# Kernel tuning notes

Measured on AMD Instinct MI355X. Metric: run time of the kernel, lower is better.

Reference implementation:

```python
import jax, jax.numpy as jnp
import numpy as np

NEG_SLOPE = 0.2  # PyG GATConv default negative_slope


def _gat_conv(x, edge_index, W, att_src, att_dst, bias, heads, out_ch, concat):
    """PyG-style GATConv with add_self_loops=False, shared src/dst lin.
    x: [N, F_in], edge_index: [2, E] (row 0 = src j, row 1 = dst i).
    W: [F_in, heads*out_ch]; att_src/att_dst: [heads, out_ch]; bias: [heads*out_ch] or [out_ch].
    """
    N = x.shape[0]
    src, dst = edge_index[0], edge_index[1]
    h = (x @ W).reshape(N, heads, out_ch)                      # [N, H, C]
    a_src = jnp.einsum('nhc,hc->nh', h, att_src)               # [N, H]
    a_dst = jnp.einsum('nhc,hc->nh', h, att_dst)               # [N, H]
    e = a_src[src] + a_dst[dst]                                # [E, H]
    e = jnp.where(e > 0, e, NEG_SLOPE * e)                     # leaky_relu
    # segment softmax over edges sharing the same destination
    m = jax.ops.segment_max(e, dst, num_segments=N)            # [N, H]
    e = jnp.exp(e - m[dst])                                    # [E, H]
    s = jax.ops.segment_sum(e, dst, num_segments=N)            # [N, H]
    alpha = e / (s[dst] + 1e-16)                               # [E, H]
    msg = h[src] * alpha[:, :, None]                           # [E, H, C]
    out = jax.ops.segment_sum(msg, dst, num_segments=N)        # [N, H, C]
    if concat:
        out = out.reshape(N, heads * out_ch)
    else:
        out = out.mean(axis=1)
    return out + bias


def setup_inputs() -> dict:
    key = jax.random.key(0)
    ks = jax.random.split(key, 12)
    N, E = 100000, 1600000
    dinp, dhid, dout, heads = 128, 32, 128, 4
    x = jax.random.normal(ks[0], (N, dinp), dtype=jnp.float32)
    a = jax.random.randint(ks[1], (2, E), 0, N, dtype=jnp.int64)
    s1 = 1.0 / np.sqrt(dinp)
    s2 = 1.0 / np.sqrt(dhid * heads)
    return {
        'x': x,
        'a': a,
        'W1': jax.random.normal(ks[2], (dinp, heads * dhid), dtype=jnp.float32) * s1,
        'att_src1': jax.random.normal(ks[3], (heads, dhid), dtype=jnp.float32) * s1,
        'att_dst1': jax.random.normal(ks[4], (heads, dhid), dtype=jnp.float32) * s1,
        'b1': jnp.zeros((heads * dhid,), dtype=jnp.float32),
        'W2': jax.random.normal(ks[5], (heads * dhid, dout), dtype=jnp.float32) * s2,
        'att_src2': jax.random.normal(ks[6], (1, dout), dtype=jnp.float32) * s2,
        'att_dst2': jax.random.normal(ks[7], (1, dout), dtype=jnp.float32) * s2,
        'b2': jnp.zeros((dout,), dtype=jnp.float32),
    }


def reference(x, a, W1, att_src1, att_dst1, b1, W2, att_src2, att_dst2, b2):
    heads, dhid, dout = 4, 32, 128
    h = _gat_conv(x, a, W1, att_src1, att_dst1, b1, heads, dhid, concat=True)
    h = jax.nn.elu(h)
    out = _gat_conv(h, a, W2, att_src2, att_dst2, b2, 1, dout, concat=False)
    return jax.nn.elu(out)
```

## Files before the change

### kernel.cpp

```cpp
#include <hip/hip_runtime.h>
#include <hip/hip_fp16.h>
#include <math.h>


typedef _Float16 f16x8 __attribute__((ext_vector_type(8)));
typedef float    f32x4 __attribute__((ext_vector_type(4)));


__global__ __launch_bounds__(256) void k_hist(const int* __restrict__ dst,
                                              int* __restrict__ bcnt, int E, int NBUCK) {
    __shared__ int lh[1024];
    int t = threadIdx.x;
    for (int i = t; i < NBUCK; i += 256) lh[i] = 0;
    __syncthreads();
    for (int e = blockIdx.x * 256 + t; e < E; e += gridDim.x * 256)
        atomicAdd(&lh[dst[e] >> 7], 1);
    __syncthreads();
    for (int i = t; i < NBUCK; i += 256) {
        int c = lh[i];
        if (c) atomicAdd(&bcnt[i], c);
    }
}

__global__ void k_bscan(const int* __restrict__ bcnt, int* __restrict__ bbase,
                        int* __restrict__ bcur, int* __restrict__ off,
                        int NBUCK, int N, int E) {
    __shared__ int sd[1024];
    int t = threadIdx.x;
    int v = (t < NBUCK) ? bcnt[t] : 0;
    sd[t] = v; __syncthreads();
    for (int ofs = 1; ofs < 1024; ofs <<= 1) {
        int w = (t >= ofs) ? sd[t - ofs] : 0;
        __syncthreads();
        sd[t] += w;
        __syncthreads();
    }
    if (t < NBUCK) { int ex = sd[t] - v; bbase[t] = ex; bcur[t] = ex; }
    if (t == 0) { bbase[NBUCK] = E; off[N] = E; }
}

__global__ __launch_bounds__(256) void k_binscatter(
    const int* __restrict__ src, const int* __restrict__ dst,
    int* __restrict__ bcur, int* __restrict__ tmp, int E, int NBUCK) {
    __shared__ int lh[1024], lbase[1024];
    int t = threadIdx.x;
    for (int i = t; i < NBUCK; i += 256) lh[i] = 0;
    __syncthreads();
    int tbeg = blockIdx.x * 8192;
    int tend = tbeg + 8192; if (tend > E) tend = E;
    for (int e = tbeg + t; e < tend; e += 256) atomicAdd(&lh[dst[e] >> 7], 1);
    __syncthreads();
    for (int i = t; i < NBUCK; i += 256) {
        int c = lh[i];
        lbase[i] = c ? atomicAdd(&bcur[i], c) : 0;
        lh[i] = 0;
    }
    __syncthreads();
    for (int e = tbeg + t; e < tend; e += 256) {
        int d = dst[e];
        int b = d >> 7;
        int r = atomicAdd(&lh[b], 1);
        tmp[lbase[b] + r] = (src[e] << 7) | (d & 127);
    }
}

__global__ __launch_bounds__(256) void k_bsort(
    const int* __restrict__ tmp, const int* __restrict__ bbase,
    int* __restrict__ off, int* __restrict__ esrc, int N) {
    __shared__ int h[128], hs[128], cur[128];
    int b = blockIdx.x, t = threadIdx.x;
    int base = bbase[b];
    int cnt  = bbase[b + 1] - base;
    int node0 = b << 7;
    if (t < 128) h[t] = 0;
    __syncthreads();
    for (int i = t; i < cnt; i += 256) atomicAdd(&h[tmp[base + i] & 127], 1);
    __syncthreads();
    if (t < 128) hs[t] = h[t];
    __syncthreads();
    for (int ofs = 1; ofs < 128; ofs <<= 1) {
        int w = (t < 128 && t >= ofs) ? hs[t - ofs] : 0;
        __syncthreads();
        if (t < 128) hs[t] += w;
        __syncthreads();
    }
    if (t < 128) {
        int ex = hs[t] - h[t];
        if (node0 + t < N) off[node0 + t] = base + ex;
        cur[t] = base + ex;
    }
    __syncthreads();
    for (int i = t; i < cnt; i += 256) {
        int p = tmp[base + i];
        int pos = atomicAdd(&cur[p & 127], 1);
        esrc[pos] = p >> 7;
    }
}


template <int H, typename TI>
__global__ __launch_bounds__(256, 2) void k_gemm_mfma(
    const TI* __restrict__ X, const float* __restrict__ Wg,
    const float* __restrict__ att_s, const float* __restrict__ att_d,
    __half* __restrict__ Y, float* __restrict__ as_, float* __restrict__ ad_, int N)
{
    __shared__ _Float16 Wh[128 * 128];
    __shared__ _Float16 Xh[64][136];
    const int t = threadIdx.x;
    const int lane = t & 63;
    const int wv = t >> 6;
    const int m = lane & 15;
    const int q = lane >> 4;

    for (int i = t; i < 128 * 128 / 4; i += 256) {
        float4 w4 = ((const float4*)Wg)[i];
        _Float16* d = &Wh[i * 4];
        d[0] = (_Float16)w4.x; d[1] = (_Float16)w4.y;
        d[2] = (_Float16)w4.z; d[3] = (_Float16)w4.w;
    }
    __syncthreads();

    f16x8 bfr[8][4];
#pragma unroll
    for (int nt = 0; nt < 8; nt++) {
#pragma unroll
        for (int ks = 0; ks < 4; ks++) {
            f16x8 b;
#pragma unroll
            for (int j = 0; j < 8; j++)
                b[j] = Wh[(ks * 32 + q * 8 + j) * 128 + nt * 16 + m];
            bfr[nt][ks] = b;
        }
    }
    float atts_v[8], attd_v[8];
#pragma unroll
    for (int nt = 0; nt < 8; nt++) {
        atts_v[nt] = att_s[nt * 16 + m];
        attd_v[nt] = att_d[nt * 16 + m];
    }

    for (int base = blockIdx.x * 64; base < N; base += gridDim.x * 64) {
        for (int i = t; i < 1024; i += 256) {
            int r = i >> 4, c8 = i & 15;
            int gr = base + r;
            _Float16* d = &Xh[r][c8 * 8];
            if (gr < N) {
                if constexpr (sizeof(TI) == 4) {
                    const float4* s = (const float4*)((const float*)X + (size_t)gr * 128 + c8 * 8);
                    float4 x0 = s[0], x1 = s[1];
                    d[0] = (_Float16)x0.x; d[1] = (_Float16)x0.y;
                    d[2] = (_Float16)x0.z; d[3] = (_Float16)x0.w;
                    d[4] = (_Float16)x1.x; d[5] = (_Float16)x1.y;
                    d[6] = (_Float16)x1.z; d[7] = (_Float16)x1.w;
                } else {
                    *(uint4*)d = *(const uint4*)((const __half*)X + (size_t)gr * 128 + c8 * 8);
                }
            } else {
                uint4 z; z.x = 0; z.y = 0; z.z = 0; z.w = 0;
                *(uint4*)d = z;
            }
        }
        __syncthreads();

        const int rowb = base + wv * 16;
        f32x4 acc[8];
#pragma unroll
        for (int nt = 0; nt < 8; nt++) { acc[nt][0] = 0.f; acc[nt][1] = 0.f; acc[nt][2] = 0.f; acc[nt][3] = 0.f; }
#pragma unroll
        for (int ks = 0; ks < 4; ks++) {
            f16x8 af = *(const f16x8*)&Xh[wv * 16 + m][ks * 32 + q * 8];
#pragma unroll
            for (int nt = 0; nt < 8; nt++)
                acc[nt] = __builtin_amdgcn_mfma_f32_16x16x32_f16(af, bfr[nt][ks], acc[nt], 0, 0, 0);
        }

#pragma unroll
        for (int nt = 0; nt < 8; nt++) {
#pragma unroll
            for (int i = 0; i < 4; i++) {
                int r = rowb + q * 4 + i;
                if (r < N) Y[(size_t)r * 128 + nt * 16 + m] = __float2half(acc[nt][i]);
            }
        }

        if (H == 4) {
            float ph[4][4], pdv[4][4];
#pragma unroll
            for (int h = 0; h < 4; h++)
#pragma unroll
                for (int i = 0; i < 4; i++) {
                    ph[h][i]  = acc[2 * h][i] * atts_v[2 * h] + acc[2 * h + 1][i] * atts_v[2 * h + 1];
                    pdv[h][i] = acc[2 * h][i] * attd_v[2 * h] + acc[2 * h + 1][i] * attd_v[2 * h + 1];
                }
#pragma unroll
            for (int lvl = 0; lvl < 4; lvl++) {
                const int msk = 1 << lvl;
#pragma unroll
                for (int h = 0; h < 4; h++)
#pragma unroll
                    for (int i = 0; i < 4; i++) {
                        ph[h][i]  += __shfl_xor(ph[h][i], msk, 64);
                        pdv[h][i] += __shfl_xor(pdv[h][i], msk, 64);
                    }
            }
            if (m == 0) {
#pragma unroll
                for (int i = 0; i < 4; i++) {
                    int r = rowb + q * 4 + i;
                    if (r < N) {
#pragma unroll
                        for (int h = 0; h < 4; h++) {
                            as_[(size_t)r * 4 + h] = ph[h][i];
                            ad_[(size_t)r * 4 + h] = pdv[h][i];
                        }
                    }
                }
            }
        } else {
            float ps[4], pdv[4];
#pragma unroll
            for (int i = 0; i < 4; i++) {
                float s = 0.f, dsum = 0.f;
#pragma unroll
                for (int nt = 0; nt < 8; nt++) {
                    s    += acc[nt][i] * atts_v[nt];
                    dsum += acc[nt][i] * attd_v[nt];
                }
                ps[i] = s; pdv[i] = dsum;
            }
#pragma unroll
            for (int lvl = 0; lvl < 4; lvl++) {
                const int msk = 1 << lvl;
#pragma unroll
                for (int i = 0; i < 4; i++) {
                    ps[i]  += __shfl_xor(ps[i], msk, 64);
                    pdv[i] += __shfl_xor(pdv[i], msk, 64);
                }
            }
            if (m == 0) {
#pragma unroll
                for (int i = 0; i < 4; i++) {
                    int r = rowb + q * 4 + i;
                    if (r < N) { as_[r] = ps[i]; ad_[r] = pdv[i]; }
                }
            }
        }
        __syncthreads();
    }
}


template <int H, typename TO>
__global__ __launch_bounds__(256) void k_agg(
    const __half* __restrict__ feat,
    const float* __restrict__ asrc,
    const float* __restrict__ adst,
    const int*   __restrict__ off,
    const int*   __restrict__ esrc,
    const float* __restrict__ bias,
    TO*          __restrict__ out,
    int N)
{
    __shared__ __attribute__((aligned(16))) int   sj[4][64];
    __shared__ __attribute__((aligned(16))) float sp[4][64 * H];

    int wave = threadIdx.x >> 6;
    int lane = threadIdx.x & 63;
    int node = (blockIdx.x * 256 + threadIdx.x) >> 6;
    if (node >= N) return;
    int beg = off[node], end = off[node + 1];

    float adst_i[H];
#pragma unroll
    for (int h = 0; h < H; h++) adst_i[h] = adst[(size_t)node * H + h];

    const int g    = lane >> 4;
    const int sub  = lane & 15;
    const int head = (H == 4) ? (sub >> 2) : 0;
    const __half* fb = feat + sub * 8;

    float o[8];
#pragma unroll
    for (int k = 0; k < 8; k++) o[k] = 0.f;
    float ssum = 0.f;

    for (int cbeg = beg; cbeg < end; cbeg += 64) {
        int cnt = end - cbeg; if (cnt > 64) cnt = 64;
        if (lane < cnt) {
            int j = esrc[cbeg + lane];
            sj[wave][lane] = j;
            if (H == 4) {
                float4 av = *(const float4*)(asrc + (size_t)j * 4);
                float e;
                e = av.x + adst_i[0]; e = e > 0.f ? e : 0.2f * e; sp[wave][0 * 64 + lane] = __expf(e);
                e = av.y + adst_i[1]; e = e > 0.f ? e : 0.2f * e; sp[wave][1 * 64 + lane] = __expf(e);
                e = av.z + adst_i[2]; e = e > 0.f ? e : 0.2f * e; sp[wave][2 * 64 + lane] = __expf(e);
                e = av.w + adst_i[3]; e = e > 0.f ? e : 0.2f * e; sp[wave][3 * 64 + lane] = __expf(e);
            } else {
                float e = asrc[j] + adst_i[0];
                e = e > 0.f ? e : 0.2f * e;
                sp[wave][lane] = __expf(e);
            }
        }
        asm volatile("s_waitcnt lgkmcnt(0)" ::: "memory");

        for (int b0 = 0; b0 < cnt; b0 += 16) {
            float aa[4]; uint4 hv[4];
#pragma unroll
            for (int u = 0; u < 4; u++) {
                int e  = b0 + 4 * u + g;
                bool ok = e < cnt;
                int ec = ok ? e : 0;
                int j  = sj[wave][ec];
                aa[u]  = ok ? sp[wave][head * 64 + ec] : 0.f;
                hv[u]  = *(const uint4*)(fb + (size_t)j * 128);
            }
#pragma unroll
            for (int u = 0; u < 4; u++) {
                const __half* hp = (const __half*)&hv[u];
                ssum += aa[u];
#pragma unroll
                for (int k = 0; k < 8; k++)
                    o[k] = fmaf(aa[u], __half2float(hp[k]), o[k]);
            }
        }
    }

#pragma unroll
    for (int k = 0; k < 8; k++) {
        o[k] += __shfl_xor(o[k], 16, 64);
        o[k] += __shfl_xor(o[k], 32, 64);
    }
    ssum += __shfl_xor(ssum, 16, 64);
    ssum += __shfl_xor(ssum, 32, 64);

    if (g == 0) {
        float inv = 1.f / (ssum + 1e-16f);
        float r[8];
#pragma unroll
        for (int k = 0; k < 8; k++) {
            r[k] = o[k] * inv + bias[sub * 8 + k];
            float er = __expf(r[k]) - 1.0f;
            r[k] = r[k] > 0.f ? r[k] : er;
        }
        if constexpr (sizeof(TO) == 2) {
            __half2 hh[4];
#pragma unroll
            for (int p = 0; p < 4; p++) hh[p] = __floats2half2_rn(r[2 * p], r[2 * p + 1]);
            *(uint4*)((__half*)out + (size_t)node * 128 + sub * 8) = *(const uint4*)hh;
        } else {
            float4 v0 = make_float4(r[0], r[1], r[2], r[3]);
            float4 v1 = make_float4(r[4], r[5], r[6], r[7]);
            *(float4*)((float*)out + (size_t)node * 128 + sub * 8)     = v0;
            *(float4*)((float*)out + (size_t)node * 128 + sub * 8 + 4) = v1;
        }
    }
}


extern "C" void kernel_launch(void* const* d_in, const int* in_sizes, int n_in,
                              void* d_out, int out_size, void* d_ws, size_t ws_size,
                              hipStream_t stream)
{
    const float* x    = (const float*)d_in[0];
    const int*   a    = (const int*)  d_in[1];
    const float* W1   = (const float*)d_in[2];
    const float* as1w = (const float*)d_in[3];
    const float* ad1w = (const float*)d_in[4];
    const float* b1   = (const float*)d_in[5];
    const float* W2   = (const float*)d_in[6];
    const float* as2w = (const float*)d_in[7];
    const float* ad2w = (const float*)d_in[8];
    const float* b2   = (const float*)d_in[9];

    const int N = in_sizes[0] / 128;
    const int E = in_sizes[1] / 2;
    const int* srcA = a;
    const int* dstA = a + E;
    const int NBUCK = (N + 127) >> 7;

    char* ws = (char*)d_ws;
    size_t o = 0;
    auto alloc = [&](size_t bytes) -> void* {
        void* p = ws + o;
        o += (bytes + 255) & ~(size_t)255;
        return p;
    };
    __half* hbuf  = (__half*)alloc((size_t)N * 128 * 2);
    __half* hact  = (__half*)alloc((size_t)N * 128 * 2);
    float*  as1   = (float*) alloc((size_t)N * 4 * 4);
    float*  ad1   = (float*) alloc((size_t)N * 4 * 4);
    float*  as2   = (float*) alloc((size_t)N * 4);
    float*  ad2   = (float*) alloc((size_t)N * 4);
    int*    off   = (int*)   alloc((size_t)(N + 1) * 4);
    int*    esrc  = (int*)   alloc((size_t)E * 4);
    int*    tmp   = (int*)   alloc((size_t)E * 4);
    int*    bcnt  = (int*)   alloc(1024 * 4);
    int*    bbase = (int*)   alloc(1025 * 4);
    int*    bcur  = (int*)   alloc(1024 * 4);

    hipMemsetAsync(bcnt, 0, (size_t)NBUCK * 4, stream);
    k_hist<<<256, 256, 0, stream>>>(dstA, bcnt, E, NBUCK);
    k_bscan<<<1, 1024, 0, stream>>>(bcnt, bbase, bcur, off, NBUCK, N, E);
    k_binscatter<<<(E + 8191) / 8192, 256, 0, stream>>>(srcA, dstA, bcur, tmp, E, NBUCK);
    k_bsort<<<NBUCK, 256, 0, stream>>>(tmp, bbase, off, esrc, N);

    k_gemm_mfma<4, float><<<512, 256, 0, stream>>>(x, W1, as1w, ad1w, hbuf, as1, ad1, N);
    k_agg<4, __half><<<(N + 3) / 4, 256, 0, stream>>>(hbuf, as1, ad1, off, esrc, b1, hact, N);

    k_gemm_mfma<1, __half><<<512, 256, 0, stream>>>(hact, W2, as2w, ad2w, hbuf, as2, ad2, N);
    k_agg<1, float><<<(N + 3) / 4, 256, 0, stream>>>(hbuf, as2, ad2, off, esrc, b2, (float*)d_out, N);
}
```

Measured before the change: 358.2 us.

## Keep GEMM weight fragments in LDS and vectorize aggregation edge loop

The GEMM kernel stops holding all 32 weight fragments in registers. It instead stores them pre-swizzled in LDS in MFMA fragment layout and reads them per tile, which lowers register pressure. That allows three blocks per CU and a larger grid. The aggregation kernel's inner loop now loads four contiguous edge indices and weights with vector LDS reads and processes four gathered rows per thread, with a separate tail path. The cost is extra LDS traffic on every GEMM tile, and the tail handling changes how edges are assigned to threads.

Measured after the change: 347.8 us. -2.9%, faster.

```diff
diff --git a/kernel.cpp b/kernel.cpp
--- a/kernel.cpp
+++ b/kernel.cpp
@@ -99,12 +99,12 @@
 
 
 template <int H, typename TI>
-__global__ __launch_bounds__(256, 2) void k_gemm_mfma(
+__global__ __launch_bounds__(256, 3) void k_gemm_mfma(
     const TI* __restrict__ X, const float* __restrict__ Wg,
     const float* __restrict__ att_s, const float* __restrict__ att_d,
     __half* __restrict__ Y, float* __restrict__ as_, float* __restrict__ ad_, int N)
 {
-    __shared__ _Float16 Wh[128 * 128];
+    __shared__ _Float16 Wf[8][4][512];
     __shared__ _Float16 Xh[64][136];
     const int t = threadIdx.x;
     const int lane = t & 63;
@@ -112,32 +112,25 @@
     const int m = lane & 15;
     const int q = lane >> 4;
 
-    for (int i = t; i < 128 * 128 / 4; i += 256) {
-        float4 w4 = ((const float4*)Wg)[i];
-        _Float16* d = &Wh[i * 4];
-        d[0] = (_Float16)w4.x; d[1] = (_Float16)w4.y;
-        d[2] = (_Float16)w4.z; d[3] = (_Float16)w4.w;
-    }
-    __syncthreads();
-
-    f16x8 bfr[8][4];
-#pragma unroll
-    for (int nt = 0; nt < 8; nt++) {
-#pragma unroll
-        for (int ks = 0; ks < 4; ks++) {
-            f16x8 b;
-#pragma unroll
-            for (int j = 0; j < 8; j++)
-                b[j] = Wh[(ks * 32 + q * 8 + j) * 128 + nt * 16 + m];
-            bfr[nt][ks] = b;
-        }
-    }
+    for (int f = t; f < 2048; f += 256) {
+        int nt = f >> 8, ks = (f >> 6) & 3, ls = f & 63;
+        int qq = ls >> 4, mm = ls & 15;
+        int col = nt * 16 + mm;
+        int k0  = ks * 32 + qq * 8;
+        f16x8 frag;
+#pragma unroll
+        for (int j = 0; j < 8; j++)
+            frag[j] = (_Float16)Wg[(size_t)(k0 + j) * 128 + col];
+        *(f16x8*)&Wf[nt][ks][ls * 8] = frag;
+    }
+
     float atts_v[8], attd_v[8];
 #pragma unroll
     for (int nt = 0; nt < 8; nt++) {
         atts_v[nt] = att_s[nt * 16 + m];
         attd_v[nt] = att_d[nt * 16 + m];
     }
+    __syncthreads();
 
     for (int base = blockIdx.x * 64; base < N; base += gridDim.x * 64) {
         for (int i = t; i < 1024; i += 256) {
@@ -163,15 +156,26 @@
         __syncthreads();
 
         const int rowb = base + wv * 16;
+
+        f16x8 af[4];
+#pragma unroll
+        for (int ks = 0; ks < 4; ks++)
+            af[ks] = *(const f16x8*)&Xh[wv * 16 + m][ks * 32 + q * 8];
+
         f32x4 acc[8];
 #pragma unroll
         for (int nt = 0; nt < 8; nt++) { acc[nt][0] = 0.f; acc[nt][1] = 0.f; acc[nt][2] = 0.f; acc[nt][3] = 0.f; }
-#pragma unroll
-        for (int ks = 0; ks < 4; ks++) {
-            f16x8 af = *(const f16x8*)&Xh[wv * 16 + m][ks * 32 + q * 8];
-#pragma unroll
-            for (int nt = 0; nt < 8; nt++)
-                acc[nt] = __builtin_amdgcn_mfma_f32_16x16x32_f16(af, bfr[nt][ks], acc[nt], 0, 0, 0);
+
+#pragma unroll
+        for (int nt = 0; nt < 8; nt++) {
+            f16x8 b0v = *(const f16x8*)&Wf[nt][0][lane * 8];
+            f16x8 b1v = *(const f16x8*)&Wf[nt][1][lane * 8];
+            f16x8 b2v = *(const f16x8*)&Wf[nt][2][lane * 8];
+            f16x8 b3v = *(const f16x8*)&Wf[nt][3][lane * 8];
+            acc[nt] = __builtin_amdgcn_mfma_f32_16x16x32_f16(af[0], b0v, acc[nt], 0, 0, 0);
+            acc[nt] = __builtin_amdgcn_mfma_f32_16x16x32_f16(af[1], b1v, acc[nt], 0, 0, 0);
+            acc[nt] = __builtin_amdgcn_mfma_f32_16x16x32_f16(af[2], b2v, acc[nt], 0, 0, 0);
+            acc[nt] = __builtin_amdgcn_mfma_f32_16x16x32_f16(af[3], b3v, acc[nt], 0, 0, 0);
         }
 
 #pragma unroll
@@ -304,13 +308,34 @@
         }
         asm volatile("s_waitcnt lgkmcnt(0)" ::: "memory");
 
-        for (int b0 = 0; b0 < cnt; b0 += 16) {
+        const int fullc = cnt & ~15;
+        for (int b0 = 0; b0 < fullc; b0 += 16) {
+            int4   j4 = *(const int4*)  &sj[wave][b0 + 4 * g];
+            float4 a4 = *(const float4*)&sp[wave][head * 64 + b0 + 4 * g];
+            uint4 hv0 = *(const uint4*)(fb + (size_t)j4.x * 128);
+            uint4 hv1 = *(const uint4*)(fb + (size_t)j4.y * 128);
+            uint4 hv2 = *(const uint4*)(fb + (size_t)j4.z * 128);
+            uint4 hv3 = *(const uint4*)(fb + (size_t)j4.w * 128);
+            ssum += (a4.x + a4.y) + (a4.z + a4.w);
+            const __half* h0 = (const __half*)&hv0;
+            const __half* h1 = (const __half*)&hv1;
+            const __half* h2 = (const __half*)&hv2;
+            const __half* h3 = (const __half*)&hv3;
+#pragma unroll
+            for (int k = 0; k < 8; k++) {
+                float v = fmaf(a4.x, __half2float(h0[k]), o[k]);
+                v = fmaf(a4.y, __half2float(h1[k]), v);
+                v = fmaf(a4.z, __half2float(h2[k]), v);
+                o[k] = fmaf(a4.w, __half2float(h3[k]), v);
+            }
+        }
+        if (fullc < cnt) {
             float aa[4]; uint4 hv[4];
 #pragma unroll
             for (int u = 0; u < 4; u++) {
-                int e  = b0 + 4 * u + g;
+                int e  = fullc + 4 * g + u;
                 bool ok = e < cnt;
-                int ec = ok ? e : 0;
+                int ec = ok ? e : fullc;
                 int j  = sj[wave][ec];
                 aa[u]  = ok ? sp[wave][head * 64 + ec] : 0.f;
                 hv[u]  = *(const uint4*)(fb + (size_t)j * 128);
@@ -405,9 +430,9 @@
     k_binscatter<<<(E + 8191) / 8192, 256, 0, stream>>>(srcA, dstA, bcur, tmp, E, NBUCK);
     k_bsort<<<NBUCK, 256, 0, stream>>>(tmp, bbase, off, esrc, N);
 
-    k_gemm_mfma<4, float><<<512, 256, 0, stream>>>(x, W1, as1w, ad1w, hbuf, as1, ad1, N);
+    k_gemm_mfma<4, float><<<768, 256, 0, stream>>>(x, W1, as1w, ad1w, hbuf, as1, ad1, N);
     k_agg<4, __half><<<(N + 3) / 4, 256, 0, stream>>>(hbuf, as1, ad1, off, esrc, b1, hact, N);
 
-    k_gemm_mfma<1, __half><<<512, 256, 0, stream>>>(hact, W2, as2w, ad2w, hbuf, as2, ad2, N);
+    k_gemm_mfma<1, __half><<<768, 256, 0, stream>>>(hact, W2, as2w, ad2w, hbuf, as2, ad2, N);
     k_agg<1, float><<<(N + 3) / 4, 256, 0, stream>>>(hbuf, as2, ad2, off, esrc, b2, (float*)d_out, N);
 }
```
